# Performance work log

Measured on AMD Instinct MI355X. Metric: run time of the kernel, lower is better.

Reference implementation:

```python
import jax, jax.numpy as jnp
import numpy as np
from jax import lax

NUM_CLASSES = 102
IN_CAPS = 2592
IN_DIM = 8
OUT_DIM = 16
ROUTINGS = 3
IMG = 112

def squash(s, axis=-1, eps=1e-8):
    sq = jnp.sum(s * s, axis=axis, keepdims=True)
    return (sq / (1.0 + sq)) * s / jnp.sqrt(sq + eps)

def conv2d(x, w, b, stride):
    y = lax.conv_general_dilated(x, w, (stride, stride), 'VALID',
                                 dimension_numbers=('NCHW', 'OIHW', 'NCHW'))
    return y + b[None, :, None, None]

def setup_inputs() -> dict:
    key = jax.random.key(0)
    ks = jax.random.split(key, 12)
    B = 32
    x = jax.random.normal(ks[0], (B, 3, IMG, IMG), jnp.float32)
    targets = jax.random.randint(ks[1], (B,), 0, NUM_CLASSES)
    conv1_w = jax.random.normal(ks[2], (256, 3, 11, 11), jnp.float32) * 0.02
    conv1_b = jnp.zeros((256,), jnp.float32)
    pc_w = jax.random.normal(ks[3], (256, 256, 9, 9), jnp.float32) * 0.02
    pc_b = jnp.zeros((256,), jnp.float32)
    W = jax.random.normal(ks[4], (NUM_CLASSES, IN_CAPS, OUT_DIM, IN_DIM), jnp.float32) * 0.01
    fc1_w = jax.random.normal(ks[5], (NUM_CLASSES * OUT_DIM, 512), jnp.float32) * 0.02
    fc1_b = jnp.zeros((512,), jnp.float32)
    fc2_w = jax.random.normal(ks[6], (512, 1024), jnp.float32) * 0.02
    fc2_b = jnp.zeros((1024,), jnp.float32)
    fc3_w = jax.random.normal(ks[7], (1024, 3 * IMG * IMG), jnp.float32) * 0.02
    fc3_b = jnp.zeros((3 * IMG * IMG,), jnp.float32)
    return dict(x=x, targets=targets, conv1_w=conv1_w, conv1_b=conv1_b,
                pc_w=pc_w, pc_b=pc_b, W=W,
                fc1_w=fc1_w, fc1_b=fc1_b, fc2_w=fc2_w, fc2_b=fc2_b,
                fc3_w=fc3_w, fc3_b=fc3_b)

def reference(x, targets, conv1_w, conv1_b, pc_w, pc_b, W,
              fc1_w, fc1_b, fc2_w, fc2_b, fc3_w, fc3_b):
    B = x.shape[0]
    # conv backbone: [B,3,112,112] -> [B,256,34,34]
    feat = jax.nn.relu(conv2d(x, conv1_w, conv1_b, 3))
    # primary caps conv: -> [B,256,9,9] -> [B,2592,8], squash
    pc = conv2d(feat, pc_w, pc_b, 3)
    u = squash(pc.reshape(B, IN_CAPS, IN_DIM))
    # prediction vectors: [B, O, N, D_out]
    x_hat = jnp.einsum('ondi,bni->bond', W, u)
    x_hat_sg = lax.stop_gradient(x_hat)
    b = jnp.zeros((B, NUM_CLASSES, IN_CAPS), x.dtype)
    v = None
    for it in range(ROUTINGS):
        c = jax.nn.softmax(b, axis=1)  # couple over out caps
        xh = x_hat if it == ROUTINGS - 1 else x_hat_sg
        s = jnp.einsum('bon,bond->bod', c, xh)
        v = squash(s)
        if it < ROUTINGS - 1:
            b = b + jnp.einsum('bond,bod->bon', xh, v)
    # reconstruction: mask by target class capsule
    mask = jax.nn.one_hot(targets, NUM_CLASSES, dtype=v.dtype)
    h = (v * mask[:, :, None]).reshape(B, NUM_CLASSES * OUT_DIM)
    h = jax.nn.relu(h @ fc1_w + fc1_b)
    h = jax.nn.relu(h @ fc2_w + fc2_b)
    recon = jax.nn.sigmoid(h @ fc3_w + fc3_b).reshape(B, 3, IMG, IMG)
    return (v, recon)
```

## Files before the change

kernel.cpp:

```cpp
#include <hip/hip_runtime.h>
#include <hip/hip_fp16.h>
#include <math.h>

#define B32   32
#define OCLS  102
#define NCAPS 2592

#define OFF_FEAT   0u
#define OFF_WQ2    0u
#define OFF_C1WT   10027008u
#define OFF_PCWQ   10119936u
#define OFF_PCP    15428352u
#define OFF_WQ     15428352u
#define OFF_U2     26045184u
#define OFF_CT     26708736u
#define OFF_FC3P   26045184u
#define OFF_S      30938880u
#define OFF_V0     30991104u
#define OFF_V1     31043328u
#define OFF_VSQ    31095552u
#define OFF_H1     31108608u
#define OFF_H2T    31124992u

typedef __attribute__((ext_vector_type(8))) short short8;
typedef __attribute__((ext_vector_type(4))) float f32x4;
typedef long long i64;

__device__ __forceinline__ unsigned short f2b(float f) {
  union { float f; unsigned u; } v; v.f = f;
  unsigned r = v.u + 0x7fffu + ((v.u >> 16) & 1u);
  return (unsigned short)(r >> 16);
}

__device__ __forceinline__ unsigned f2q_fast(float x) {
  union { float f; unsigned u; } v; v.f = x;
  unsigned s = (v.u >> 24) & 0x80u;
  unsigned au = v.u & 0x7fffffffu;
  if (au < 0x3c800000u) return s;
  if (au >= 0x43e00000u) return s | 0x7eu;
  unsigned r = au + 0x7ffffu + ((au >> 20) & 1u);
  unsigned e = (r >> 23) - 120u;
  unsigned m = (r >> 20) & 7u;
  return s | (e << 3) | m;
}

__device__ __forceinline__ unsigned fp8pair(float a, float b) {
#if __has_builtin(__builtin_amdgcn_cvt_pk_fp8_f32)
  return (unsigned)__builtin_amdgcn_cvt_pk_fp8_f32(a, b, 0, false) & 0xffffu;
#else
  return f2q_fast(a) | (f2q_fast(b) << 8);
#endif
}

__global__ void k_mkC1B(const float* __restrict__ conv1_w,
                        unsigned short* __restrict__ C1WB) {
  int co = blockIdx.x;
  int t = threadIdx.x;
#pragma unroll
  for (int ci = 0; ci < 3; ++ci) {
    float v = (t < 121) ? conv1_w[co * 363 + ci * 121 + t] : 0.f;
    C1WB[(ci * 256 + co) * 128 + t] = f2b(v);
  }
}

__global__ void k_mkBq(const float* __restrict__ pc_w, unsigned char* __restrict__ PCWQ) {
  int co = blockIdx.x;
  for (int e = threadIdx.x; e < 20736; e += 256) {
    int ci = e / 81, tap = e - ci * 81;
    PCWQ[(size_t)ci * 26624 + co * 104 + tap] =
        (unsigned char)f2q_fast(pc_w[(size_t)co * 20736 + e] * 64.f);
  }
  int ci = threadIdx.x;
  for (int tap = 81; tap < 104; ++tap)
    PCWQ[(size_t)ci * 26624 + co * 104 + tap] = 0;
}

__global__ __launch_bounds__(256) void k_mkW2(const float* __restrict__ W,
                                              unsigned char* __restrict__ Wq2,
                                              unsigned char* __restrict__ Wq) {
  __shared__ unsigned char sq[32 * 128];
  int t = threadIdx.x;
  size_t base = (size_t)blockIdx.x * 4096;
  const float4* src = (const float4*)(W + base + (size_t)t * 16);
  float4 f0 = src[0], f1 = src[1], f2 = src[2], f3 = src[3];
  float v[16] = {f0.x, f0.y, f0.z, f0.w, f1.x, f1.y, f1.z, f1.w,
                 f2.x, f2.y, f2.z, f2.w, f3.x, f3.y, f3.z, f3.w};
  unsigned words[4];
#pragma unroll
  for (int j = 0; j < 4; ++j)
    words[j] = fp8pair(v[4 * j] * 64.f, v[4 * j + 1] * 64.f) |
               (fp8pair(v[4 * j + 2] * 64.f, v[4 * j + 3] * 64.f) << 16);
  *(uint4*)(Wq2 + base + (size_t)t * 16) =
      make_uint4(words[0], words[1], words[2], words[3]);

  int r = t >> 3, seg = t & 7;
#pragma unroll
  for (int e = 0; e < 16; ++e) {
    unsigned byte = (words[e >> 2] >> ((e & 3) * 8)) & 0xffu;
    int idx = seg * 16 + e, d = idx >> 3, i = idx & 7;
    sq[r * 128 + i * 16 + d] = (unsigned char)byte;
  }
  __syncthreads();
  *(uint4*)(Wq + base + (size_t)t * 16) = ((const uint4*)sq)[t];
}

__global__ __launch_bounds__(256) void k_c1m(const float* __restrict__ x,
                                             const unsigned short* __restrict__ C1WB,
                                             const float* __restrict__ bias,
                                             float* __restrict__ feat2) {
  __shared__ unsigned short sh[48 * 128 + 256 * 128];
  unsigned short* lA = sh;
  unsigned short* lB = sh + 48 * 128;
  float* obuf = (float*)(sh + 48 * 128);

  int bx = blockIdx.x;
  int b = bx / 34, ho = bx % 34;
  int t = threadIdx.x;
  int lane = t & 63, wv = t >> 6;
  int l15 = lane & 15, lh = lane >> 4;
  int rx = l15 & 7;

  {
    uint4 zz = make_uint4(0, 0, 0, 0);
    uint4* z = (uint4*)lA;
    for (int i = t; i < 48 * 128 / 8; i += 256) z[i] = zz;
  }
  __syncthreads();

  f32x4 acc[3][4];
#pragma unroll
  for (int mf = 0; mf < 3; ++mf)
#pragma unroll
    for (int nf = 0; nf < 4; ++nf) acc[mf][nf] = (f32x4){0.f, 0.f, 0.f, 0.f};

#pragma unroll 1
  for (int ci = 0; ci < 3; ++ci) {
    {
      const uint4* Bsrc = (const uint4*)(C1WB + ci * 32768);
#pragma unroll
      for (int i = 0; i < 16; ++i) {
        int f = i * 256 + t;
        int row = f >> 4, cu = f & 15;
        ((uint4*)lB)[row * 16 + (cu ^ (row & 7))] = Bsrc[f];
      }
    }
    for (int tk = t; tk < 374; tk += 256) {
      int kh = tk / 34, wo = tk - kh * 34;
      const float* src = x + ((size_t)(b * 3 + ci) * 112 + ho * 3 + kh) * 112 + wo * 3;
#pragma unroll
      for (int j = 0; j < 11; ++j) {
        int tap = kh * 11 + j;
        int cu = tap >> 3;
        lA[wo * 128 + (((cu ^ (wo & 7)) << 3) | (tap & 7))] = f2b(src[j]);
      }
    }
    __syncthreads();

#pragma unroll
    for (int s = 0; s < 4; ++s) {
      int cub = ((s * 4 + lh) ^ rx) << 3;
      short8 a0 = *(const short8*)(lA + (0 + l15) * 128 + cub);
      short8 a1 = *(const short8*)(lA + (16 + l15) * 128 + cub);
      short8 a2 = *(const short8*)(lA + (32 + l15) * 128 + cub);
      short8 b0 = *(const short8*)(lB + (wv * 64 + 0 + l15) * 128 + cub);
      short8 b1 = *(const short8*)(lB + (wv * 64 + 16 + l15) * 128 + cub);
      short8 b2 = *(const short8*)(lB + (wv * 64 + 32 + l15) * 128 + cub);
      short8 b3 = *(const short8*)(lB + (wv * 64 + 48 + l15) * 128 + cub);
      acc[0][0] = __builtin_amdgcn_mfma_f32_16x16x32_bf16(a0, b0, acc[0][0], 0, 0, 0);
      acc[0][1] = __builtin_amdgcn_mfma_f32_16x16x32_bf16(a0, b1, acc[0][1], 0, 0, 0);
      acc[0][2] = __builtin_amdgcn_mfma_f32_16x16x32_bf16(a0, b2, acc[0][2], 0, 0, 0);
      acc[0][3] = __builtin_amdgcn_mfma_f32_16x16x32_bf16(a0, b3, acc[0][3], 0, 0, 0);
      acc[1][0] = __builtin_amdgcn_mfma_f32_16x16x32_bf16(a1, b0, acc[1][0], 0, 0, 0);
      acc[1][1] = __builtin_amdgcn_mfma_f32_16x16x32_bf16(a1, b1, acc[1][1], 0, 0, 0);
      acc[1][2] = __builtin_amdgcn_mfma_f32_16x16x32_bf16(a1, b2, acc[1][2], 0, 0, 0);
      acc[1][3] = __builtin_amdgcn_mfma_f32_16x16x32_bf16(a1, b3, acc[1][3], 0, 0, 0);
      acc[2][0] = __builtin_amdgcn_mfma_f32_16x16x32_bf16(a2, b0, acc[2][0], 0, 0, 0);
      acc[2][1] = __builtin_amdgcn_mfma_f32_16x16x32_bf16(a2, b1, acc[2][1], 0, 0, 0);
      acc[2][2] = __builtin_amdgcn_mfma_f32_16x16x32_bf16(a2, b2, acc[2][2], 0, 0, 0);
      acc[2][3] = __builtin_amdgcn_mfma_f32_16x16x32_bf16(a2, b3, acc[2][3], 0, 0, 0);
    }
    __syncthreads();
  }

  float bv[4];
#pragma unroll
  for (int nf = 0; nf < 4; ++nf) bv[nf] = bias[wv * 64 + nf * 16 + l15];
#pragma unroll
  for (int mf = 0; mf < 3; ++mf)
#pragma unroll
    for (int nf = 0; nf < 4; ++nf)
#pragma unroll
      for (int r = 0; r < 4; ++r) {
        int wo = mf * 16 + lh * 4 + r;
        if (wo < 36)
          obuf[(wv * 64 + nf * 16 + l15) * 36 + wo] = fmaxf(acc[mf][nf][r] + bv[nf], 0.f);
      }
  __syncthreads();
  float4* dst = (float4*)(feat2 + (size_t)bx * 9216);
  const float4* srcb = (const float4*)obuf;
#pragma unroll
  for (int i = 0; i < 9; ++i) dst[i * 256 + t] = srcb[i * 256 + t];
}

__device__ __forceinline__ void pc_gather8(const float* __restrict__ feat2,
                                           unsigned char* __restrict__ dstbuf,
                                           int mb, int ci, int t) {
  for (int task = t; task < 576; task += 256) {
    int m = task / 9, kh = task - m * 9;
    int gm = mb * 64 + m;
    if (gm < 2592) {
      int b = gm / 81, p = gm - b * 81;
      int ho = p / 9, wo = p - ho * 9;
      const float* src = feat2 + ((size_t)(b * 34 + ho * 3 + kh) * 256 + ci) * 36 + wo * 3;
      unsigned char* dst = dstbuf + m * 104 + kh * 9;
      unsigned p01 = fp8pair(src[0], src[1]);
      unsigned p23 = fp8pair(src[2], src[3]);
      unsigned p45 = fp8pair(src[4], src[5]);
      unsigned p67 = fp8pair(src[6], src[7]);
      unsigned p8  = fp8pair(src[8], 0.f);
      dst[0] = p01; dst[1] = p01 >> 8;
      dst[2] = p23; dst[3] = p23 >> 8;
      dst[4] = p45; dst[5] = p45 >> 8;
      dst[6] = p67; dst[7] = p67 >> 8;
      dst[8] = p8;
    }
  }
}

__global__ __launch_bounds__(256, 3) void k_pc4(const float* __restrict__ feat2,
                                                const unsigned char* __restrict__ PCWQ,
                                                float* __restrict__ pcp) {
  __shared__ unsigned char lA[2][64 * 104];

  int mb = blockIdx.x, kc = blockIdx.y;
  int t = threadIdx.x;
  int lane = t & 63, wv = t >> 6;
  int l15 = lane & 15, lh = lane >> 4;

  {
    uint4 zz = make_uint4(0, 0, 0, 0);
    uint4* z = (uint4*)lA;
    for (int i = t; i < 2 * 64 * 104 / 16; i += 256) z[i] = zz;
  }
  __syncthreads();
  pc_gather8(feat2, lA[0], mb, kc * 16, t);
  __syncthreads();

  f32x4 acc[4][4];
#pragma unroll
  for (int mf = 0; mf < 4; ++mf)
#pragma unroll
    for (int nf = 0; nf < 4; ++nf) acc[mf][nf] = (f32x4){0.f, 0.f, 0.f, 0.f};

#pragma unroll 1
  for (int cil = 0; cil < 16; ++cil) {
    int ci = kc * 16 + cil;
    int cur = cil & 1;

    i64 bfr[4][3];
    const unsigned char* Bbase = PCWQ + (size_t)ci * 26624 + (wv * 64 + l15) * 104 + lh * 8;
#pragma unroll
    for (int nf = 0; nf < 4; ++nf)
#pragma unroll
      for (int s = 0; s < 3; ++s)
        bfr[nf][s] = *(const i64*)(Bbase + nf * 16 * 104 + s * 32);

    if (cil < 15) pc_gather8(feat2, lA[cur ^ 1], mb, ci + 1, t);

    const unsigned char* arow = lA[cur] + l15 * 104 + lh * 8;
#pragma unroll
    for (int s = 0; s < 3; ++s) {
      i64 a0 = *(const i64*)(arow + s * 32);
      i64 a1 = *(const i64*)(arow + 16 * 104 + s * 32);
      i64 a2 = *(const i64*)(arow + 32 * 104 + s * 32);
      i64 a3 = *(const i64*)(arow + 48 * 104 + s * 32);
      acc[0][0] = __builtin_amdgcn_mfma_f32_16x16x32_fp8_fp8(a0, bfr[0][s], acc[0][0], 0, 0, 0);
      acc[0][1] = __builtin_amdgcn_mfma_f32_16x16x32_fp8_fp8(a0, bfr[1][s], acc[0][1], 0, 0, 0);
      acc[0][2] = __builtin_amdgcn_mfma_f32_16x16x32_fp8_fp8(a0, bfr[2][s], acc[0][2], 0, 0, 0);
      acc[0][3] = __builtin_amdgcn_mfma_f32_16x16x32_fp8_fp8(a0, bfr[3][s], acc[0][3], 0, 0, 0);
      acc[1][0] = __builtin_amdgcn_mfma_f32_16x16x32_fp8_fp8(a1, bfr[0][s], acc[1][0], 0, 0, 0);
      acc[1][1] = __builtin_amdgcn_mfma_f32_16x16x32_fp8_fp8(a1, bfr[1][s], acc[1][1], 0, 0, 0);
      acc[1][2] = __builtin_amdgcn_mfma_f32_16x16x32_fp8_fp8(a1, bfr[2][s], acc[1][2], 0, 0, 0);
      acc[1][3] = __builtin_amdgcn_mfma_f32_16x16x32_fp8_fp8(a1, bfr[3][s], acc[1][3], 0, 0, 0);
      acc[2][0] = __builtin_amdgcn_mfma_f32_16x16x32_fp8_fp8(a2, bfr[0][s], acc[2][0], 0, 0, 0);
      acc[2][1] = __builtin_amdgcn_mfma_f32_16x16x32_fp8_fp8(a2, bfr[1][s], acc[2][1], 0, 0, 0);
      acc[2][2] = __builtin_amdgcn_mfma_f32_16x16x32_fp8_fp8(a2, bfr[2][s], acc[2][2], 0, 0, 0);
      acc[2][3] = __builtin_amdgcn_mfma_f32_16x16x32_fp8_fp8(a2, bfr[3][s], acc[2][3], 0, 0, 0);
      acc[3][0] = __builtin_amdgcn_mfma_f32_16x16x32_fp8_fp8(a3, bfr[0][s], acc[3][0], 0, 0, 0);
      acc[3][1] = __builtin_amdgcn_mfma_f32_16x16x32_fp8_fp8(a3, bfr[1][s], acc[3][1], 0, 0, 0);
      acc[3][2] = __builtin_amdgcn_mfma_f32_16x16x32_fp8_fp8(a3, bfr[2][s], acc[3][2], 0, 0, 0);
      acc[3][3] = __builtin_amdgcn_mfma_f32_16x16x32_fp8_fp8(a3, bfr[3][s], acc[3][3], 0, 0, 0);
    }
    __syncthreads();
  }

#pragma unroll
  for (int mf = 0; mf < 4; ++mf) {
    int gm = mb * 64 + mf * 16 + lh * 4;
    if (gm < 2592) {
      float* dst = pcp + (size_t)kc * 663552 + (size_t)gm * 256 + wv * 64 + l15;
#pragma unroll
      for (int nf = 0; nf < 4; ++nf)
#pragma unroll
        for (int r = 0; r < 4; ++r)
          dst[(size_t)r * 256 + nf * 16] = acc[mf][nf][r];
    }
  }
}

__global__ __launch_bounds__(256) void k_rs(const float* __restrict__ pcp,
                                            const float* __restrict__ pcb,
                                            float* __restrict__ u2) {
  __shared__ float tile[81 * 65];
  int b = blockIdx.x;
  int cog = blockIdx.y;
  int c0 = cog * 64;
  int t = threadIdx.x;

  for (int e = t; e < 5184; e += 256) {
    int p = e >> 6, col = e & 63;
    const float* base = pcp + (size_t)(b * 81 + p) * 256 + c0 + col;
    float s = 0.f;
#pragma unroll
    for (int c = 0; c < 16; ++c) s += base[(size_t)c * 663552];
    tile[p * 65 + col] = pcb[c0 + col] + s * 0.015625f;
  }
  __syncthreads();

  for (int cap = t; cap < 648; cap += 256) {
    float v[8];
    float sq = 0.f;
#pragma unroll
    for (int i = 0; i < 8; ++i) {
      int g = cap * 8 + i;
      int col = g / 81, p = g - col * 81;
      v[i] = tile[p * 65 + col];
      sq += v[i] * v[i];
    }
    float sc = (sq / (1.f + sq)) / sqrtf(sq + 1e-8f);
    int n = cog * 648 + cap;
    float4* dst = (float4*)(u2 + ((size_t)b * 2592 + n) * 8);
    dst[0] = make_float4(v[0] * sc, v[1] * sc, v[2] * sc, v[3] * sc);
    dst[1] = make_float4(v[4] * sc, v[5] * sc, v[6] * sc, v[7] * sc);
  }
}

__global__ __launch_bounds__(128) void k_A2(const unsigned char* __restrict__ Wq,
                                            const float* __restrict__ u2,
                                            const unsigned char* __restrict__ vq,
                                            __half* __restrict__ cT) {
  __shared__ __half Eld[102 * 2 * 2 * 32];
  int nb = blockIdx.x;
  int t = threadIdx.x, wv = t >> 6, lane = t & 63;
  int l15 = lane & 15, g = lane >> 4;
  int n0 = nb * 4 + 2 * wv;
  int nl = g >> 1, ih = (g & 1) * 4;

  float4 u0 = *(const float4*)(u2 + (((size_t)l15 * 2592 + n0 + nl) * 8 + ih));
  float4 u1 = *(const float4*)(u2 + (((size_t)(l15 + 16) * 2592 + n0 + nl) * 8 + ih));

  int nlA = l15 >> 3, iA = l15 & 7;
  const unsigned char* Ap = Wq + (((size_t)(n0 + nlA)) * 8 + iA) * 16 + (g & 1) * 8;
  const unsigned char* B0p = vq + (size_t)l15 * 16 + (g & 1) * 8;
  bool act = (g < 2);

  float den0 = 0.f, den1 = 0.f;
#pragma unroll 2
  for (int o = 0; o < 102; ++o) {
    i64 a = 0, b0 = 0, b1 = 0;
    if (act) {
      a  = *(const i64*)(Ap + (size_t)o * 331776);
      b0 = *(const i64*)(B0p + (size_t)o * 512);
      b1 = *(const i64*)(B0p + (size_t)o * 512 + 256);
    }
    f32x4 d0 = {0.f, 0.f, 0.f, 0.f}, d1 = {0.f, 0.f, 0.f, 0.f};
    d0 = __builtin_amdgcn_mfma_f32_16x16x32_fp8_fp8(a, b0, d0, 0, 0, 0);
    d1 = __builtin_amdgcn_mfma_f32_16x16x32_fp8_fp8(a, b1, d1, 0, 0, 0);
    float p0 = d0[0] * u0.x + d0[1] * u0.y + d0[2] * u0.z + d0[3] * u0.w;
    float p1 = d1[0] * u1.x + d1[1] * u1.y + d1[2] * u1.z + d1[3] * u1.w;
    p0 += __shfl_xor(p0, 16);
    p1 += __shfl_xor(p1, 16);
    p0 *= 1.52587890625e-05f;
    p1 *= 1.52587890625e-05f;
    float e0 = __expf(p0), e1 = __expf(p1);
    den0 += e0; den1 += e1;
    if ((g & 1) == 0) {
      int base = (o * 2 + wv) * 64 + (g >> 1) * 16 + l15;
      Eld[base] = __float2half(e0);
      Eld[base + 32] = __float2half(e1);
    }
  }
  float r0 = 1.0f / den0, r1 = 1.0f / den1;
  if ((g & 1) == 0) {
    for (int o = 0; o < 102; ++o) {
      int base = (o * 2 + wv) * 64 + (g >> 1) * 16 + l15;
      float c0 = __half2float(Eld[base]) * r0;
      float c1 = __half2float(Eld[base + 32]) * r1;
      __half* dst = cT + ((size_t)o * 2592 + n0 + (g >> 1)) * 32 + l15;
      dst[0] = __float2half(c0);
      dst[16] = __float2half(c1);
    }
  }
}

__device__ __forceinline__ i64 cu_pack8(float c, float4 a, float4 b) {
  union { unsigned u[2]; i64 v; } r;
  r.u[0] = fp8pair(c * a.x, c * a.y) | (fp8pair(c * a.z, c * a.w) << 16);
  r.u[1] = fp8pair(c * b.x, c * b.y) | (fp8pair(c * b.z, c * b.w) << 16);
  return r.v;
}

template <bool HASC>
__global__ __launch_bounds__(256) void k_B3(const unsigned char* __restrict__ Wq2,
                                            const float* __restrict__ u2,
                                            const __half* __restrict__ cT,
                                            float* __restrict__ s) {
  int o = blockIdx.x, kc = blockIdx.y;
  int t = threadIdx.x, lane = t & 63, wv = t >> 6;
  int l15 = lane & 15, h = lane >> 4;

  f32x4 acc0 = {0.f, 0.f, 0.f, 0.f}, acc1 = {0.f, 0.f, 0.f, 0.f};

#pragma unroll 1
  for (int st = wv; st < 81; st += 4) {
    int n = kc * 324 + st * 4 + h;
    i64 aq = *(const i64*)(Wq2 + (((size_t)o * 2592 + n) * 16 + l15) * 8);

    const float4* u0p = (const float4*)(u2 + ((size_t)l15 * 2592 + n) * 8);
    float4 u0a = u0p[0], u0b = u0p[1];
    const float4* u1p = (const float4*)(u2 + ((size_t)(l15 + 16) * 2592 + n) * 8);
    float4 u1a = u1p[0], u1b = u1p[1];

    float c0 = 16.0f, c1 = 16.0f;
    if (HASC) {
      const __half* cp = cT + ((size_t)o * 2592 + n) * 32;
      c0 = 16.0f * __half2float(cp[l15]);
      c1 = 16.0f * __half2float(cp[l15 + 16]);
    }
    i64 b0 = cu_pack8(c0, u0a, u0b);
    i64 b1 = cu_pack8(c1, u1a, u1b);

    acc0 = __builtin_amdgcn_mfma_f32_16x16x32_fp8_fp8(aq, b0, acc0, 0, 0, 0);
    acc1 = __builtin_amdgcn_mfma_f32_16x16x32_fp8_fp8(aq, b1, acc1, 0, 0, 0);
  }

#pragma unroll
  for (int r = 0; r < 4; ++r) {
    atomicAdd(s + ((size_t)l15 * 102 + o) * 16 + h * 4 + r, acc0[r]);
    atomicAdd(s + ((size_t)(l15 + 16) * 102 + o) * 16 + h * 4 + r, acc1[r]);
  }
}

__global__ void k_R(const float* __restrict__ s, float scale,
                    float* __restrict__ vout, const float* __restrict__ addin,
                    unsigned char* __restrict__ vsq) {
  int t = blockIdx.x * 256 + threadIdx.x;
  if (t >= 3264) return;
  const float* sp = s + t * 16;
  float r[16];
  float sq = 0.f;
#pragma unroll
  for (int d = 0; d < 16; ++d) {
    r[d] = sp[d] * scale;
    sq += r[d] * r[d];
  }
  float sc = (sq / (1.f + sq)) / sqrtf(sq + 1e-8f);
  float vv[16];
#pragma unroll
  for (int d = 0; d < 16; ++d) {
    vv[d] = r[d] * sc;
    vout[t * 16 + d] = vv[d];
  }
  if (vsq) {
    int b = t / 102, o = t - b * 102;
    float w[16];
#pragma unroll
    for (int d = 0; d < 16; ++d)
      w[d] = (addin ? (addin[t * 16 + d] + vv[d]) : vv[d]) * 1024.f;
    unsigned words[4];
#pragma unroll
    for (int q = 0; q < 4; ++q)
      words[q] = fp8pair(w[4 * q], w[4 * q + 1]) | (fp8pair(w[4 * q + 2], w[4 * q + 3]) << 16);
    *(uint4*)(vsq + ((size_t)o * 32 + b) * 16) =
        make_uint4(words[0], words[1], words[2], words[3]);
  }
}

__global__ void k_fc1(const float* __restrict__ v2, const int* __restrict__ tgt,
                      const float* __restrict__ w1, const float* __restrict__ b1,
                      float* __restrict__ h1) {
  int j = blockIdx.x * 128 + threadIdx.x;
  int bq = blockIdx.y;
#pragma unroll
  for (int bi = 0; bi < 4; ++bi) {
    int b = bq * 4 + bi;
    int tb = tgt[b];
    float acc = b1[j];
    const float* vv = v2 + (b * 102 + tb) * 16;
    const float* wr = w1 + (tb * 16) * 512 + j;
#pragma unroll
    for (int d = 0; d < 16; ++d) acc += vv[d] * wr[d * 512];
    h1[b * 512 + j] = fmaxf(acc, 0.f);
  }
}

__global__ void k_fc2(const float* __restrict__ h1, const float* __restrict__ w2,
                      const float* __restrict__ b2, float* __restrict__ h2T) {
  int j = blockIdx.x * 128 + threadIdx.x;
  int bq = blockIdx.y;
  float acc[4];
#pragma unroll
  for (int bi = 0; bi < 4; ++bi) acc[bi] = b2[j];
  for (int k = 0; k < 512; ++k) {
    float wv = w2[k * 1024 + j];
#pragma unroll
    for (int bi = 0; bi < 4; ++bi) acc[bi] += h1[(bq * 4 + bi) * 512 + k] * wv;
  }
  float4 o;
  o.x = fmaxf(acc[0], 0.f); o.y = fmaxf(acc[1], 0.f);
  o.z = fmaxf(acc[2], 0.f); o.w = fmaxf(acc[3], 0.f);
  *(float4*)(h2T + j * 32 + bq * 4) = o;
}

__global__ void k_fc3a(const float* __restrict__ h2T, const float* __restrict__ w3,
                       float* __restrict__ p) {
  int j = blockIdx.x * 128 + threadIdx.x;
  int ky = blockIdx.y;
  float acc[32];
#pragma unroll
  for (int i = 0; i < 32; ++i) acc[i] = 0.f;
  int k0 = ky * 256;
  for (int k = k0; k < k0 + 256; ++k) {
    float wv = w3[(size_t)k * 37632 + j];
    const float4* hp = (const float4*)(h2T + k * 32);
#pragma unroll
    for (int q = 0; q < 8; ++q) {
      float4 h = hp[q];
      acc[q * 4 + 0] += h.x * wv; acc[q * 4 + 1] += h.y * wv;
      acc[q * 4 + 2] += h.z * wv; acc[q * 4 + 3] += h.w * wv;
    }
  }
#pragma unroll
  for (int i = 0; i < 32; ++i)
    p[((size_t)ky * 32 + i) * 37632 + j] = acc[i];
}

__global__ void k_fc3b(const float* __restrict__ p, const float* __restrict__ b3,
                       float* __restrict__ out) {
  int j = blockIdx.x * 256 + threadIdx.x;
  float bv = b3[j];
#pragma unroll 1
  for (int b = 0; b < 32; ++b) {
    float s = bv + p[(size_t)b * 37632 + j] + p[(size_t)(32 + b) * 37632 + j] +
              p[(size_t)(64 + b) * 37632 + j] + p[(size_t)(96 + b) * 37632 + j];
    out[52224 + (size_t)b * 37632 + j] = 1.0f / (1.0f + __expf(-s));
  }
}

extern "C" void kernel_launch(void* const* d_in, const int* in_sizes, int n_in,
                              void* d_out, int out_size, void* d_ws, size_t ws_size,
                              hipStream_t stream) {
  const float* x       = (const float*)d_in[0];
  const int*   targets = (const int*)d_in[1];
  const float* conv1_w = (const float*)d_in[2];
  const float* conv1_b = (const float*)d_in[3];
  const float* pc_w    = (const float*)d_in[4];
  const float* pc_b    = (const float*)d_in[5];
  const float* W       = (const float*)d_in[6];
  const float* fc1_w   = (const float*)d_in[7];
  const float* fc1_b   = (const float*)d_in[8];
  const float* fc2_w   = (const float*)d_in[9];
  const float* fc2_b   = (const float*)d_in[10];
  const float* fc3_w   = (const float*)d_in[11];
  const float* fc3_b   = (const float*)d_in[12];
  float* out = (float*)d_out;
  float* ws = (float*)d_ws;

  float* FEAT2 = ws + OFF_FEAT;
  unsigned short* C1WB = (unsigned short*)(ws + OFF_C1WT);
  unsigned char* PCWQ = (unsigned char*)(ws + OFF_PCWQ);
  float* PCP  = ws + OFF_PCP;
  float* U2   = ws + OFF_U2;
  unsigned char* WQ2 = (unsigned char*)(ws + OFF_WQ2);
  unsigned char* WQ  = (unsigned char*)(ws + OFF_WQ);
  __half* CT  = (__half*)(ws + OFF_CT);
  float* FC3P = ws + OFF_FC3P;
  float* S    = ws + OFF_S;
  float* V0   = ws + OFF_V0;
  float* V1   = ws + OFF_V1;
  unsigned char* VSQ = (unsigned char*)(ws + OFF_VSQ);
  float* H1   = ws + OFF_H1;
  float* H2T  = ws + OFF_H2T;

  k_mkC1B<<<dim3(256), 128, 0, stream>>>(conv1_w, C1WB);
  k_mkBq<<<dim3(256), 256, 0, stream>>>(pc_w, PCWQ);

  k_c1m<<<dim3(1088), 256, 0, stream>>>(x, C1WB, conv1_b, FEAT2);

  k_pc4<<<dim3(41, 16), 256, 0, stream>>>(FEAT2, PCWQ, PCP);
  k_rs<<<dim3(32, 4), 256, 0, stream>>>(PCP, pc_b, U2);

  k_mkW2<<<dim3(8262), 256, 0, stream>>>(W, WQ2, WQ);

  hipMemsetAsync(S, 0, 52224 * sizeof(float), stream);
  k_B3<false><<<dim3(102, 8), 256, 0, stream>>>(WQ2, U2, nullptr, S);
  k_R<<<dim3(13), 256, 0, stream>>>(S, 1.0f / (102.0f * 1024.0f), V0, nullptr, VSQ);

  k_A2<<<dim3(648), 128, 0, stream>>>(WQ, U2, VSQ, CT);
  hipMemsetAsync(S, 0, 52224 * sizeof(float), stream);
  k_B3<true><<<dim3(102, 8), 256, 0, stream>>>(WQ2, U2, CT, S);
  k_R<<<dim3(13), 256, 0, stream>>>(S, 1.0f / 1024.0f, V1, V0, VSQ);

  k_A2<<<dim3(648), 128, 0, stream>>>(WQ, U2, VSQ, CT);
  hipMemsetAsync(S, 0, 52224 * sizeof(float), stream);
  k_B3<true><<<dim3(102, 8), 256, 0, stream>>>(WQ2, U2, CT, S);
  k_R<<<dim3(13), 256, 0, stream>>>(S, 1.0f / 1024.0f, out, nullptr, nullptr);

  k_fc1<<<dim3(4, 8), 128, 0, stream>>>(out, targets, fc1_w, fc1_b, H1);
  k_fc2<<<dim3(8, 8), 128, 0, stream>>>(H1, fc2_w, fc2_b, H2T);
  k_fc3a<<<dim3(294, 4), 128, 0, stream>>>(H2T, fc3_w, FC3P);
  k_fc3b<<<dim3(147), 256, 0, stream>>>(FC3P, fc3_b, out);
}
```

Measured before the change: 641.0 us.

## Increase grid parallelism in conv kernels, store fp16 partials, fold S zeroing into squash

```diff
diff --git a/kernel.cpp b/kernel.cpp
--- a/kernel.cpp
+++ b/kernel.cpp
@@ -108,12 +108,13 @@
                                              const unsigned short* __restrict__ C1WB,
                                              const float* __restrict__ bias,
                                              float* __restrict__ feat2) {
-  __shared__ unsigned short sh[48 * 128 + 256 * 128];
+  __shared__ unsigned short sh[48 * 128 + 128 * 128];
   unsigned short* lA = sh;
   unsigned short* lB = sh + 48 * 128;
   float* obuf = (float*)(sh + 48 * 128);
 
   int bx = blockIdx.x;
+  int hf = blockIdx.y;
   int b = bx / 34, ho = bx % 34;
   int t = threadIdx.x;
   int lane = t & 63, wv = t >> 6;
@@ -127,18 +128,18 @@
   }
   __syncthreads();
 
-  f32x4 acc[3][4];
+  f32x4 acc[3][2];
 #pragma unroll
   for (int mf = 0; mf < 3; ++mf)
 #pragma unroll
-    for (int nf = 0; nf < 4; ++nf) acc[mf][nf] = (f32x4){0.f, 0.f, 0.f, 0.f};
+    for (int nf = 0; nf < 2; ++nf) acc[mf][nf] = (f32x4){0.f, 0.f, 0.f, 0.f};
 
 #pragma unroll 1
   for (int ci = 0; ci < 3; ++ci) {
     {
-      const uint4* Bsrc = (const uint4*)(C1WB + ci * 32768);
-#pragma unroll
-      for (int i = 0; i < 16; ++i) {
+      const uint4* Bsrc = (const uint4*)(C1WB + ci * 32768 + hf * 16384);
+#pragma unroll
+      for (int i = 0; i < 8; ++i) {
         int f = i * 256 + t;
         int row = f >> 4, cu = f & 15;
         ((uint4*)lB)[row * 16 + (cu ^ (row & 7))] = Bsrc[f];
@@ -162,44 +163,35 @@
       short8 a0 = *(const short8*)(lA + (0 + l15) * 128 + cub);
       short8 a1 = *(const short8*)(lA + (16 + l15) * 128 + cub);
       short8 a2 = *(const short8*)(lA + (32 + l15) * 128 + cub);
-      short8 b0 = *(const short8*)(lB + (wv * 64 + 0 + l15) * 128 + cub);
-      short8 b1 = *(const short8*)(lB + (wv * 64 + 16 + l15) * 128 + cub);
-      short8 b2 = *(const short8*)(lB + (wv * 64 + 32 + l15) * 128 + cub);
-      short8 b3 = *(const short8*)(lB + (wv * 64 + 48 + l15) * 128 + cub);
+      short8 b0 = *(const short8*)(lB + (wv * 32 + 0 + l15) * 128 + cub);
+      short8 b1 = *(const short8*)(lB + (wv * 32 + 16 + l15) * 128 + cub);
       acc[0][0] = __builtin_amdgcn_mfma_f32_16x16x32_bf16(a0, b0, acc[0][0], 0, 0, 0);
       acc[0][1] = __builtin_amdgcn_mfma_f32_16x16x32_bf16(a0, b1, acc[0][1], 0, 0, 0);
-      acc[0][2] = __builtin_amdgcn_mfma_f32_16x16x32_bf16(a0, b2, acc[0][2], 0, 0, 0);
-      acc[0][3] = __builtin_amdgcn_mfma_f32_16x16x32_bf16(a0, b3, acc[0][3], 0, 0, 0);
       acc[1][0] = __builtin_amdgcn_mfma_f32_16x16x32_bf16(a1, b0, acc[1][0], 0, 0, 0);
       acc[1][1] = __builtin_amdgcn_mfma_f32_16x16x32_bf16(a1, b1, acc[1][1], 0, 0, 0);
-      acc[1][2] = __builtin_amdgcn_mfma_f32_16x16x32_bf16(a1, b2, acc[1][2], 0, 0, 0);
-      acc[1][3] = __builtin_amdgcn_mfma_f32_16x16x32_bf16(a1, b3, acc[1][3], 0, 0, 0);
       acc[2][0] = __builtin_amdgcn_mfma_f32_16x16x32_bf16(a2, b0, acc[2][0], 0, 0, 0);
       acc[2][1] = __builtin_amdgcn_mfma_f32_16x16x32_bf16(a2, b1, acc[2][1], 0, 0, 0);
-      acc[2][2] = __builtin_amdgcn_mfma_f32_16x16x32_bf16(a2, b2, acc[2][2], 0, 0, 0);
-      acc[2][3] = __builtin_amdgcn_mfma_f32_16x16x32_bf16(a2, b3, acc[2][3], 0, 0, 0);
     }
     __syncthreads();
   }
 
-  float bv[4];
-#pragma unroll
-  for (int nf = 0; nf < 4; ++nf) bv[nf] = bias[wv * 64 + nf * 16 + l15];
+  float bv[2];
+#pragma unroll
+  for (int nf = 0; nf < 2; ++nf) bv[nf] = bias[hf * 128 + wv * 32 + nf * 16 + l15];
 #pragma unroll
   for (int mf = 0; mf < 3; ++mf)
 #pragma unroll
-    for (int nf = 0; nf < 4; ++nf)
+    for (int nf = 0; nf < 2; ++nf)
 #pragma unroll
       for (int r = 0; r < 4; ++r) {
         int wo = mf * 16 + lh * 4 + r;
         if (wo < 36)
-          obuf[(wv * 64 + nf * 16 + l15) * 36 + wo] = fmaxf(acc[mf][nf][r] + bv[nf], 0.f);
+          obuf[(wv * 32 + nf * 16 + l15) * 36 + wo] = fmaxf(acc[mf][nf][r] + bv[nf], 0.f);
       }
   __syncthreads();
-  float4* dst = (float4*)(feat2 + (size_t)bx * 9216);
+  float4* dst = (float4*)(feat2 + (size_t)bx * 9216 + hf * 4608);
   const float4* srcb = (const float4*)obuf;
-#pragma unroll
-  for (int i = 0; i < 9; ++i) dst[i * 256 + t] = srcb[i * 256 + t];
+  for (int i = t; i < 1152; i += 256) dst[i] = srcb[i];
 }
 
 __device__ __forceinline__ void pc_gather8(const float* __restrict__ feat2,
@@ -229,7 +221,7 @@
 
 __global__ __launch_bounds__(256, 3) void k_pc4(const float* __restrict__ feat2,
                                                 const unsigned char* __restrict__ PCWQ,
-                                                float* __restrict__ pcp) {
+                                                __half* __restrict__ pcp) {
   __shared__ unsigned char lA[2][64 * 104];
 
   int mb = blockIdx.x, kc = blockIdx.y;
@@ -243,7 +235,7 @@
     for (int i = t; i < 2 * 64 * 104 / 16; i += 256) z[i] = zz;
   }
   __syncthreads();
-  pc_gather8(feat2, lA[0], mb, kc * 16, t);
+  pc_gather8(feat2, lA[0], mb, kc * 8, t);
   __syncthreads();
 
   f32x4 acc[4][4];
@@ -253,8 +245,8 @@
     for (int nf = 0; nf < 4; ++nf) acc[mf][nf] = (f32x4){0.f, 0.f, 0.f, 0.f};
 
 #pragma unroll 1
-  for (int cil = 0; cil < 16; ++cil) {
-    int ci = kc * 16 + cil;
+  for (int cil = 0; cil < 8; ++cil) {
+    int ci = kc * 8 + cil;
     int cur = cil & 1;
 
     i64 bfr[4][3];
@@ -265,7 +257,7 @@
       for (int s = 0; s < 3; ++s)
         bfr[nf][s] = *(const i64*)(Bbase + nf * 16 * 104 + s * 32);
 
-    if (cil < 15) pc_gather8(feat2, lA[cur ^ 1], mb, ci + 1, t);
+    if (cil < 7) pc_gather8(feat2, lA[cur ^ 1], mb, ci + 1, t);
 
     const unsigned char* arow = lA[cur] + l15 * 104 + lh * 8;
 #pragma unroll
@@ -298,47 +290,47 @@
   for (int mf = 0; mf < 4; ++mf) {
     int gm = mb * 64 + mf * 16 + lh * 4;
     if (gm < 2592) {
-      float* dst = pcp + (size_t)kc * 663552 + (size_t)gm * 256 + wv * 64 + l15;
+      __half* dst = pcp + (size_t)kc * 663552 + (size_t)gm * 256 + wv * 64 + l15;
 #pragma unroll
       for (int nf = 0; nf < 4; ++nf)
 #pragma unroll
         for (int r = 0; r < 4; ++r)
-          dst[(size_t)r * 256 + nf * 16] = acc[mf][nf][r];
-    }
-  }
-}
-
-__global__ __launch_bounds__(256) void k_rs(const float* __restrict__ pcp,
+          dst[(size_t)r * 256 + nf * 16] = __float2half(acc[mf][nf][r]);
+    }
+  }
+}
+
+__global__ __launch_bounds__(256) void k_rs(const __half* __restrict__ pcp,
                                             const float* __restrict__ pcb,
                                             float* __restrict__ u2) {
-  __shared__ float tile[81 * 65];
+  __shared__ float tile[81 * 17];
   int b = blockIdx.x;
   int cog = blockIdx.y;
-  int c0 = cog * 64;
+  int c0 = cog * 16;
   int t = threadIdx.x;
 
-  for (int e = t; e < 5184; e += 256) {
-    int p = e >> 6, col = e & 63;
-    const float* base = pcp + (size_t)(b * 81 + p) * 256 + c0 + col;
+  for (int e = t; e < 1296; e += 256) {
+    int p = e >> 4, col = e & 15;
+    const __half* base = pcp + (size_t)(b * 81 + p) * 256 + c0 + col;
     float s = 0.f;
 #pragma unroll
-    for (int c = 0; c < 16; ++c) s += base[(size_t)c * 663552];
-    tile[p * 65 + col] = pcb[c0 + col] + s * 0.015625f;
+    for (int c = 0; c < 32; ++c) s += __half2float(base[(size_t)c * 663552]);
+    tile[p * 17 + col] = pcb[c0 + col] + s * 0.015625f;
   }
   __syncthreads();
 
-  for (int cap = t; cap < 648; cap += 256) {
+  if (t < 162) {
     float v[8];
     float sq = 0.f;
 #pragma unroll
     for (int i = 0; i < 8; ++i) {
-      int g = cap * 8 + i;
+      int g = t * 8 + i;
       int col = g / 81, p = g - col * 81;
-      v[i] = tile[p * 65 + col];
+      v[i] = tile[p * 17 + col];
       sq += v[i] * v[i];
     }
     float sc = (sq / (1.f + sq)) / sqrtf(sq + 1e-8f);
-    int n = cog * 648 + cap;
+    int n = cog * 162 + t;
     float4* dst = (float4*)(u2 + ((size_t)b * 2592 + n) * 8);
     dst[0] = make_float4(v[0] * sc, v[1] * sc, v[2] * sc, v[3] * sc);
     dst[1] = make_float4(v[4] * sc, v[5] * sc, v[6] * sc, v[7] * sc);
@@ -422,8 +414,8 @@
   f32x4 acc0 = {0.f, 0.f, 0.f, 0.f}, acc1 = {0.f, 0.f, 0.f, 0.f};
 
 #pragma unroll 1
-  for (int st = wv; st < 81; st += 4) {
-    int n = kc * 324 + st * 4 + h;
+  for (int st = wv; st < 54; st += 4) {
+    int n = kc * 216 + st * 4 + h;
     i64 aq = *(const i64*)(Wq2 + (((size_t)o * 2592 + n) * 16 + l15) * 8);
 
     const float4* u0p = (const float4*)(u2 + ((size_t)l15 * 2592 + n) * 8);
@@ -453,7 +445,7 @@
 
 __global__ void k_R(const float* __restrict__ s, float scale,
                     float* __restrict__ vout, const float* __restrict__ addin,
-                    unsigned char* __restrict__ vsq) {
+                    unsigned char* __restrict__ vsq, float* __restrict__ szero) {
   int t = blockIdx.x * 256 + threadIdx.x;
   if (t >= 3264) return;
   const float* sp = s + t * 16;
@@ -463,6 +455,10 @@
   for (int d = 0; d < 16; ++d) {
     r[d] = sp[d] * scale;
     sq += r[d] * r[d];
+  }
+  if (szero) {
+#pragma unroll
+    for (int d = 0; d < 16; ++d) szero[t * 16 + d] = 0.f;
   }
   float sc = (sq / (1.f + sq)) / sqrtf(sq + 1e-8f);
   float vv[16];
@@ -579,7 +575,7 @@
   float* FEAT2 = ws + OFF_FEAT;
   unsigned short* C1WB = (unsigned short*)(ws + OFF_C1WT);
   unsigned char* PCWQ = (unsigned char*)(ws + OFF_PCWQ);
-  float* PCP  = ws + OFF_PCP;
+  __half* PCP = (__half*)(ws + OFF_PCP);
   float* U2   = ws + OFF_U2;
   unsigned char* WQ2 = (unsigned char*)(ws + OFF_WQ2);
   unsigned char* WQ  = (unsigned char*)(ws + OFF_WQ);
@@ -595,26 +591,24 @@
   k_mkC1B<<<dim3(256), 128, 0, stream>>>(conv1_w, C1WB);
   k_mkBq<<<dim3(256), 256, 0, stream>>>(pc_w, PCWQ);
 
-  k_c1m<<<dim3(1088), 256, 0, stream>>>(x, C1WB, conv1_b, FEAT2);
-
-  k_pc4<<<dim3(41, 16), 256, 0, stream>>>(FEAT2, PCWQ, PCP);
-  k_rs<<<dim3(32, 4), 256, 0, stream>>>(PCP, pc_b, U2);
+  k_c1m<<<dim3(1088, 2), 256, 0, stream>>>(x, C1WB, conv1_b, FEAT2);
+
+  k_pc4<<<dim3(41, 32), 256, 0, stream>>>(FEAT2, PCWQ, PCP);
+  k_rs<<<dim3(32, 16), 256, 0, stream>>>(PCP, pc_b, U2);
 
   k_mkW2<<<dim3(8262), 256, 0, stream>>>(W, WQ2, WQ);
 
   hipMemsetAsync(S, 0, 52224 * sizeof(float), stream);
-  k_B3<false><<<dim3(102, 8), 256, 0, stream>>>(WQ2, U2, nullptr, S);
-  k_R<<<dim3(13), 256, 0, stream>>>(S, 1.0f / (102.0f * 1024.0f), V0, nullptr, VSQ);
+  k_B3<false><<<dim3(102, 12), 256, 0, stream>>>(WQ2, U2, nullptr, S);
+  k_R<<<dim3(13), 256, 0, stream>>>(S, 1.0f / (102.0f * 1024.0f), V0, nullptr, VSQ, S);
 
   k_A2<<<dim3(648), 128, 0, stream>>>(WQ, U2, VSQ, CT);
-  hipMemsetAsync(S, 0, 52224 * sizeof(float), stream);
-  k_B3<true><<<dim3(102, 8), 256, 0, stream>>>(WQ2, U2, CT, S);
-  k_R<<<dim3(13), 256, 0, stream>>>(S, 1.0f / 1024.0f, V1, V0, VSQ);
+  k_B3<true><<<dim3(102, 12), 256, 0, stream>>>(WQ2, U2, CT, S);
+  k_R<<<dim3(13), 256, 0, stream>>>(S, 1.0f / 1024.0f, V1, V0, VSQ, S);
 
   k_A2<<<dim3(648), 128, 0, stream>>>(WQ, U2, VSQ, CT);
-  hipMemsetAsync(S, 0, 52224 * sizeof(float), stream);
-  k_B3<true><<<dim3(102, 8), 256, 0, stream>>>(WQ2, U2, CT, S);
-  k_R<<<dim3(13), 256, 0, stream>>>(S, 1.0f / 1024.0f, out, nullptr, nullptr);
+  k_B3<true><<<dim3(102, 12), 256, 0, stream>>>(WQ2, U2, CT, S);
+  k_R<<<dim3(13), 256, 0, stream>>>(S, 1.0f / 1024.0f, out, nullptr, nullptr, nullptr);
 
   k_fc1<<<dim3(4, 8), 128, 0, stream>>>(out, targets, fc1_w, fc1_b, H1);
   k_fc2<<<dim3(8, 8), 128, 0, stream>>>(H1, fc2_w, fc2_b, H2T);
```

Result: no change. 636.0 us (-0.8%).
